# Optimization experiments

Hardware: AMD Instinct MI355X
Metric: run time of the kernel (lower is better)

## Reference

```python
import jax, jax.numpy as jnp
import numpy as np

B, S, D, H = 2, 2048, 1024, 16
DH = D // H
LN_EPS = 1e-12


def setup_inputs() -> dict:
    key = jax.random.key(0)
    ks = jax.random.split(key, 12)
    sc = 1.0 / np.sqrt(D)
    return {
        "hidden_states": jax.random.normal(ks[0], (B, S, D), jnp.float32),
        "attention_mask": jnp.zeros((B, 1, 1, S), jnp.float32),
        "Wq": jax.random.normal(ks[1], (D, D), jnp.float32) * sc,
        "bq": jnp.zeros((D,), jnp.float32),
        "Wk": jax.random.normal(ks[2], (D, D), jnp.float32) * sc,
        "bk": jnp.zeros((D,), jnp.float32),
        "Wv": jax.random.normal(ks[3], (D, D), jnp.float32) * sc,
        "bv": jnp.zeros((D,), jnp.float32),
        "Wo": jax.random.normal(ks[4], (D, D), jnp.float32) * sc,
        "bo": jnp.zeros((D,), jnp.float32),
        "ln_w": jnp.ones((D,), jnp.float32),
        "ln_b": jnp.zeros((D,), jnp.float32),
    }


def _split_heads(x):
    # [B,S,D] -> [B,H,S,DH]
    return x.reshape(B, S, H, DH).transpose(0, 2, 1, 3)


def reference(hidden_states, attention_mask, Wq, bq, Wk, bk, Wv, bv, Wo, bo, ln_w, ln_b):
    q = _split_heads(hidden_states @ Wq + bq)
    k = _split_heads(hidden_states @ Wk + bk)
    v = _split_heads(hidden_states @ Wv + bv)
    scores = jnp.einsum("bhqd,bhkd->bhqk", q, k) / np.sqrt(DH)
    scores = scores + attention_mask
    probs = jax.nn.softmax(scores, axis=-1)  # dropout prob=0 -> identity
    ctx = jnp.einsum("bhqk,bhkd->bhqd", probs, v)
    ctx = ctx.transpose(0, 2, 1, 3).reshape(B, S, D)
    # output dense + residual + LayerNorm (biased variance, per original)
    h = ctx @ Wo + bo + hidden_states
    u = h.mean(-1, keepdims=True)
    s = ((h - u) ** 2).mean(-1, keepdims=True)
    out = ln_w * ((h - u) / jnp.sqrt(s + LN_EPS)) + ln_b
    return out, probs
```

## Files before the change

### kernel.cpp

```cpp
#include <hip/hip_runtime.h>
#include <stdint.h>


typedef __attribute__((ext_vector_type(8))) short short8;
typedef __attribute__((ext_vector_type(4))) float f32x4;

__device__ __forceinline__ unsigned short f2b(float f) {
  union { float f; unsigned u; } v; v.f = f;
  unsigned u = v.u;
  return (unsigned short)((u + 0x7fffu + ((u >> 16) & 1u)) >> 16);
}

__device__ __forceinline__ float b2f(unsigned short s) {
  union { unsigned u; float f; } v;
  v.u = ((unsigned)s) << 16;
  return v.f;
}

__global__ void k_cast_hs(const float* __restrict__ x, unsigned short* __restrict__ y, int n4) {
  int i = blockIdx.x * blockDim.x + threadIdx.x;
  if (i < n4) {
    float4 v = ((const float4*)x)[i];
    ushort4 o;
    o.x = f2b(v.x); o.y = f2b(v.y); o.z = f2b(v.z); o.w = f2b(v.w);
    ((ushort4*)y)[i] = o;
  }
}

__global__ void k_transpose_cast(const float* __restrict__ Wq, const float* __restrict__ Wk,
                                 const float* __restrict__ Wv, const float* __restrict__ Wo,
                                 unsigned short* __restrict__ Tq, unsigned short* __restrict__ Tk,
                                 unsigned short* __restrict__ Tv, unsigned short* __restrict__ To) {
  __shared__ float tile[32][33];
  const float* W; unsigned short* T;
  switch (blockIdx.z) {
    case 0: W = Wq; T = Tq; break;
    case 1: W = Wk; T = Tk; break;
    case 2: W = Wv; T = Tv; break;
    default: W = Wo; T = To; break;
  }
  int n0 = blockIdx.x * 32, k0 = blockIdx.y * 32;
  int tx = threadIdx.x, ty = threadIdx.y;
#pragma unroll
  for (int j = 0; j < 4; ++j)
    tile[ty + j * 8][tx] = W[(size_t)(k0 + ty + j * 8) * 1024 + n0 + tx];
  __syncthreads();
#pragma unroll
  for (int j = 0; j < 4; ++j)
    T[(size_t)(n0 + ty + j * 8) * 1024 + k0 + tx] = f2b(tile[tx][ty + j * 8]);
}

template <int MODE>
__global__ __launch_bounds__(256) void k_gemm(const unsigned short* __restrict__ A,
                                              const unsigned short* __restrict__ Bt, int Kd,
                                              const float* __restrict__ bias,
                                              const float* __restrict__ resid,
                                              void* __restrict__ outp, float qscale) {
  __shared__ __align__(16) unsigned short Asm[128 * 32];
  __shared__ __align__(16) unsigned short Bsm[128 * 32];
  const int t = threadIdx.x, w = t >> 6, l = t & 63;
  const int m0 = blockIdx.y * 128, n0 = blockIdx.x * 128;
  const int wr = w >> 1, wc = w & 1;
  const int lr = l & 15, lg = l >> 4;

  f32x4 acc[4][4];
#pragma unroll
  for (int mi = 0; mi < 4; ++mi)
#pragma unroll
    for (int ni = 0; ni < 4; ++ni) acc[mi][ni] = (f32x4){0.f, 0.f, 0.f, 0.f};

  const int kcol = (l & 3) * 8;
  for (int kt = 0; kt < Kd / 32; ++kt) {
    const int k0 = kt * 32;
#pragma unroll
    for (int i = 0; i < 2; ++i) {
      int ra = (i * 4 + w) * 16 + (l >> 2);
      const unsigned short* ga = A + (size_t)(m0 + ra) * Kd + k0 + kcol;
      __builtin_amdgcn_global_load_lds((const __attribute__((address_space(1))) void*)ga,
                                       (__attribute__((address_space(3))) void*)((char*)Asm + (i * 4 + w) * 1024),
                                       16, 0, 0);
      const unsigned short* gb = Bt + (size_t)(n0 + ra) * Kd + k0 + kcol;
      __builtin_amdgcn_global_load_lds((const __attribute__((address_space(1))) void*)gb,
                                       (__attribute__((address_space(3))) void*)((char*)Bsm + (i * 4 + w) * 1024),
                                       16, 0, 0);
    }
    __syncthreads();
    short8 af[4], bfv[4];
#pragma unroll
    for (int mi = 0; mi < 4; ++mi)
      af[mi] = *(const short8*)&Asm[(wr * 64 + mi * 16 + lr) * 32 + lg * 8];
#pragma unroll
    for (int ni = 0; ni < 4; ++ni)
      bfv[ni] = *(const short8*)&Bsm[(wc * 64 + ni * 16 + lr) * 32 + lg * 8];
#pragma unroll
    for (int mi = 0; mi < 4; ++mi)
#pragma unroll
      for (int ni = 0; ni < 4; ++ni)
        acc[mi][ni] = __builtin_amdgcn_mfma_f32_16x16x32_bf16(af[mi], bfv[ni], acc[mi][ni], 0, 0, 0);
    __syncthreads();
  }

#pragma unroll
  for (int mi = 0; mi < 4; ++mi) {
#pragma unroll
    for (int ni = 0; ni < 4; ++ni) {
#pragma unroll
      for (int r = 0; r < 4; ++r) {
        int row = m0 + wr * 64 + mi * 16 + lg * 4 + r;
        int col = n0 + wc * 64 + ni * 16 + lr;
        float v = acc[mi][ni][r];
        if constexpr (MODE == 0) {
          v = (v + bias[col]) * qscale;
          int b = row >> 11, s = row & 2047, h = col >> 6, dh = col & 63;
          ((unsigned short*)outp)[((size_t)((b * 16 + h) * 2048 + s)) * 64 + dh] = f2b(v);
        } else if constexpr (MODE == 1) {
          v += bias[row];
          int h = row >> 6, dh = row & 63, b = col >> 11, s = col & 2047;
          ((unsigned short*)outp)[((size_t)((b * 16 + h) * 64 + dh)) * 2048 + s] = f2b(v);
        } else {
          v += bias[col] + resid[(size_t)row * 1024 + col];
          ((float*)outp)[(size_t)row * 1024 + col] = v;
        }
      }
    }
  }
}

__global__ __launch_bounds__(256, 2) void k_attn(const unsigned short* __restrict__ Q,
                                                 const unsigned short* __restrict__ K,
                                                 const unsigned short* __restrict__ VT,
                                                 const float* __restrict__ mask,
                                                 float* __restrict__ probs,
                                                 unsigned short* __restrict__ ctx) {
  __shared__ float smax[4][16];
  __shared__ float ssum[4][16];
  __shared__ __align__(16) unsigned short Pall[16][2056];
  float (*redbuf)[16][64] = (float(*)[16][64])Pall;

  const int t = threadIdx.x, w = t >> 6, l = t & 63;
  const int qb = blockIdx.x, h = blockIdx.y, b = blockIdx.z;
  const int q0 = qb * 16;
  const int lr = l & 15, lg = l >> 4;
  const size_t head = ((size_t)(b * 16 + h)) * 2048 * 64;
  const unsigned short* Qh = Q + head + (size_t)q0 * 64;
  const unsigned short* Kh = K + head;
  const unsigned short* VTh = VT + head;

  short8 aq0 = *(const short8*)(Qh + lr * 64 + lg * 8);
  short8 aq1 = *(const short8*)(Qh + lr * 64 + 32 + lg * 8);

  f32x4 sc[32];
#pragma unroll
  for (int ni = 0; ni < 32; ++ni) {
    int col = w * 512 + ni * 16 + lr;
    short8 bk0 = *(const short8*)(Kh + (size_t)col * 64 + lg * 8);
    short8 bk1 = *(const short8*)(Kh + (size_t)col * 64 + 32 + lg * 8);
    f32x4 c = (f32x4){0.f, 0.f, 0.f, 0.f};
    c = __builtin_amdgcn_mfma_f32_16x16x32_bf16(bk0, aq0, c, 0, 0, 0);
    c = __builtin_amdgcn_mfma_f32_16x16x32_bf16(bk1, aq1, c, 0, 0, 0);
    f32x4 mv = *(const f32x4*)(mask + b * 2048 + w * 512 + ni * 16 + lg * 4);
    sc[ni] = c + mv;
  }

  float vmax = -1e30f;
#pragma unroll
  for (int ni = 0; ni < 32; ++ni)
#pragma unroll
    for (int r = 0; r < 4; ++r) vmax = fmaxf(vmax, sc[ni][r]);
  vmax = fmaxf(vmax, __shfl_xor(vmax, 16));
  vmax = fmaxf(vmax, __shfl_xor(vmax, 32));
  if (l < 16) smax[w][l] = vmax;
  __syncthreads();
  float m = fmaxf(fmaxf(smax[0][lr], smax[1][lr]), fmaxf(smax[2][lr], smax[3][lr]));

  float vsum = 0.f;
#pragma unroll
  for (int ni = 0; ni < 32; ++ni)
#pragma unroll
    for (int r = 0; r < 4; ++r) {
      float p = __expf(sc[ni][r] - m);
      sc[ni][r] = p;
      vsum += p;
    }
  vsum += __shfl_xor(vsum, 16);
  vsum += __shfl_xor(vsum, 32);
  if (l < 16) ssum[w][l] = vsum;
  __syncthreads();
  float rinv = 1.f / (ssum[0][lr] + ssum[1][lr] + ssum[2][lr] + ssum[3][lr]);

#pragma unroll
  for (int ni = 0; ni < 32; ++ni) {
    float p0 = sc[ni][0] * rinv, p1 = sc[ni][1] * rinv;
    float p2 = sc[ni][2] * rinv, p3 = sc[ni][3] * rinv;
    ushort4 pk;
    pk.x = f2b(p0); pk.y = f2b(p1); pk.z = f2b(p2); pk.w = f2b(p3);
    *(ushort4*)&Pall[lr][w * 512 + ni * 16 + lg * 4] = pk;
  }
  __syncthreads();

  f32x4 cacc[4];
#pragma unroll
  for (int n = 0; n < 4; ++n) cacc[n] = (f32x4){0.f, 0.f, 0.f, 0.f};

#pragma unroll
  for (int kc = 0; kc < 16; ++kc) {
    short8 pa = *(const short8*)&Pall[lr][w * 512 + kc * 32 + lg * 8];
    size_t kg = (size_t)w * 512 + kc * 32;
#pragma unroll
    for (int n = 0; n < 4; ++n) {
      short8 bv = *(const short8*)(VTh + (size_t)(n * 16 + lr) * 2048 + kg + lg * 8);
      cacc[n] = __builtin_amdgcn_mfma_f32_16x16x32_bf16(pa, bv, cacc[n], 0, 0, 0);
    }
  }

  {
    const size_t prow0 = ((size_t)((b * 16 + h) * 2048 + q0)) * 2048;
#pragma unroll
    for (int rr = 0; rr < 4; ++rr) {
      int row = w * 4 + rr;
      float* gp = probs + prow0 + (size_t)row * 2048;
#pragma unroll
      for (int p = 0; p < 4; ++p) {
        short8 pv = *(const short8*)&Pall[row][p * 512 + l * 8];
        f32x4 o0, o1;
        o0[0] = b2f((unsigned short)pv[0]); o0[1] = b2f((unsigned short)pv[1]);
        o0[2] = b2f((unsigned short)pv[2]); o0[3] = b2f((unsigned short)pv[3]);
        o1[0] = b2f((unsigned short)pv[4]); o1[1] = b2f((unsigned short)pv[5]);
        o1[2] = b2f((unsigned short)pv[6]); o1[3] = b2f((unsigned short)pv[7]);
        f32x4* dst = (f32x4*)(gp + p * 512 + l * 8);
        __builtin_nontemporal_store(o0, dst);
        __builtin_nontemporal_store(o1, dst + 1);
      }
    }
  }
  __syncthreads();

#pragma unroll
  for (int n = 0; n < 4; ++n)
#pragma unroll
    for (int r = 0; r < 4; ++r)
      redbuf[w][lg * 4 + r][n * 16 + lr] = cacc[n][r];
  __syncthreads();

  {
    int row = t >> 4;
    int c0 = (t & 15) * 4;
    float v0 = redbuf[0][row][c0] + redbuf[1][row][c0] + redbuf[2][row][c0] + redbuf[3][row][c0];
    float v1 = redbuf[0][row][c0 + 1] + redbuf[1][row][c0 + 1] + redbuf[2][row][c0 + 1] + redbuf[3][row][c0 + 1];
    float v2 = redbuf[0][row][c0 + 2] + redbuf[1][row][c0 + 2] + redbuf[2][row][c0 + 2] + redbuf[3][row][c0 + 2];
    float v3 = redbuf[0][row][c0 + 3] + redbuf[1][row][c0 + 3] + redbuf[2][row][c0 + 3] + redbuf[3][row][c0 + 3];
    ushort4 o;
    o.x = f2b(v0); o.y = f2b(v1); o.z = f2b(v2); o.w = f2b(v3);
    *(ushort4*)(ctx + ((size_t)(b * 2048 + q0 + row)) * 1024 + h * 64 + c0) = o;
  }
}

__global__ __launch_bounds__(256) void k_ln(const float* __restrict__ hbuf, const float* __restrict__ g,
                                            const float* __restrict__ be, float* __restrict__ out) {
  __shared__ float psum[4];
  __shared__ float psq[4];
  int tok = blockIdx.x;
  int t = threadIdx.x, w = t >> 6;
  float4 v = ((const float4*)(hbuf + (size_t)tok * 1024))[t];
  float s = v.x + v.y + v.z + v.w;
  float q = v.x * v.x + v.y * v.y + v.z * v.z + v.w * v.w;
#pragma unroll
  for (int off = 32; off >= 1; off >>= 1) {
    s += __shfl_xor(s, off);
    q += __shfl_xor(q, off);
  }
  if ((t & 63) == 0) { psum[w] = s; psq[w] = q; }
  __syncthreads();
  float S = psum[0] + psum[1] + psum[2] + psum[3];
  float Qs = psq[0] + psq[1] + psq[2] + psq[3];
  float u = S * (1.f / 1024.f);
  float var = Qs * (1.f / 1024.f) - u * u;
  float rstd = rsqrtf(var + 1e-12f);
  float4 gv = ((const float4*)g)[t];
  float4 bv = ((const float4*)be)[t];
  float4 o;
  o.x = gv.x * ((v.x - u) * rstd) + bv.x;
  o.y = gv.y * ((v.y - u) * rstd) + bv.y;
  o.z = gv.z * ((v.z - u) * rstd) + bv.z;
  o.w = gv.w * ((v.w - u) * rstd) + bv.w;
  ((float4*)(out + (size_t)tok * 1024))[t] = o;
}

extern "C" void kernel_launch(void* const* d_in, const int* in_sizes, int n_in,
                              void* d_out, int out_size, void* d_ws, size_t ws_size,
                              hipStream_t stream) {
  const float* hs   = (const float*)d_in[0];
  const float* mask = (const float*)d_in[1];
  const float* Wq   = (const float*)d_in[2];
  const float* bq   = (const float*)d_in[3];
  const float* Wk   = (const float*)d_in[4];
  const float* bk   = (const float*)d_in[5];
  const float* Wv   = (const float*)d_in[6];
  const float* bv   = (const float*)d_in[7];
  const float* Wo   = (const float*)d_in[8];
  const float* bo   = (const float*)d_in[9];
  const float* lnw  = (const float*)d_in[10];
  const float* lnb  = (const float*)d_in[11];

  float* out = (float*)d_out;
  float* probs = out + (size_t)4194304;

  char* ws = (char*)d_ws;
  const size_t MB = 1u << 20;
  unsigned short* hsb = (unsigned short*)(ws + 0 * MB);
  unsigned short* TqW = (unsigned short*)(ws + 8 * MB);
  unsigned short* TkW = (unsigned short*)(ws + 10 * MB);
  unsigned short* TvW = (unsigned short*)(ws + 12 * MB);
  unsigned short* ToW = (unsigned short*)(ws + 14 * MB);
  unsigned short* Qb  = (unsigned short*)(ws + 16 * MB);
  unsigned short* Kb  = (unsigned short*)(ws + 24 * MB);
  unsigned short* VTb = (unsigned short*)(ws + 32 * MB);
  unsigned short* ctxb = (unsigned short*)(ws + 40 * MB);
  float* hbuf = (float*)(ws + 48 * MB);

  k_cast_hs<<<4096, 256, 0, stream>>>(hs, hsb, 1048576);
  k_transpose_cast<<<dim3(32, 32, 4), dim3(32, 8), 0, stream>>>(Wq, Wk, Wv, Wo, TqW, TkW, TvW, ToW);

  k_gemm<0><<<dim3(8, 32), 256, 0, stream>>>(hsb, TqW, 1024, bq, nullptr, Qb, 0.125f);
  k_gemm<0><<<dim3(8, 32), 256, 0, stream>>>(hsb, TkW, 1024, bk, nullptr, Kb, 1.0f);
  k_gemm<1><<<dim3(32, 8), 256, 0, stream>>>(TvW, hsb, 1024, bv, nullptr, VTb, 1.0f);

  k_attn<<<dim3(128, 16, 2), 256, 0, stream>>>(Qb, Kb, VTb, mask, probs, ctxb);

  k_gemm<2><<<dim3(8, 32), 256, 0, stream>>>(ctxb, ToW, 1024, bo, hs, hbuf, 1.0f);
  k_ln<<<4096, 256, 0, stream>>>(hbuf, lnw, lnb, out);
}
```

Measured before the change: 456.0 us.

## Stream P·V in staged LDS chunks to cut shared memory and raise occupancy

The attention kernel no longer keeps the full 16x2048 bf16 probability tile in LDS. Each wave in turn stages its 512-column slice into a small buffer. All waves then write that slice to the probs output and accumulate P·V for their own 16 output columns, so the cross-wave reduction buffer goes away. The launch bound rises from 2 to 8 blocks per SIMD, and the block index is remapped so neighbouring blocks span different heads and batches. This trades extra barriers and 32 packed registers per thread for much lower LDS use and higher occupancy.

```diff
diff --git a/kernel.cpp b/kernel.cpp
--- a/kernel.cpp
+++ b/kernel.cpp
@@ -126,7 +126,7 @@
   }
 }
 
-__global__ __launch_bounds__(256, 2) void k_attn(const unsigned short* __restrict__ Q,
+__global__ __launch_bounds__(256, 8) void k_attn(const unsigned short* __restrict__ Q,
                                                  const unsigned short* __restrict__ K,
                                                  const unsigned short* __restrict__ VT,
                                                  const float* __restrict__ mask,
@@ -134,11 +134,13 @@
                                                  unsigned short* __restrict__ ctx) {
   __shared__ float smax[4][16];
   __shared__ float ssum[4][16];
-  __shared__ __align__(16) unsigned short Pall[16][2056];
-  float (*redbuf)[16][64] = (float(*)[16][64])Pall;
+  __shared__ __align__(16) unsigned short Pb[16][520];
 
   const int t = threadIdx.x, w = t >> 6, l = t & 63;
-  const int qb = blockIdx.x, h = blockIdx.y, b = blockIdx.z;
+  const int i = blockIdx.x;
+  const int hp = (i & 7) * 4 + ((i >> 3) & 3);
+  const int qb = i >> 5;
+  const int h = hp & 15, b = hp >> 4;
   const int q0 = qb * 16;
   const int lr = l & 15, lg = l >> 4;
   const size_t head = ((size_t)(b * 16 + h)) * 2048 * 64;
@@ -188,70 +190,52 @@
   __syncthreads();
   float rinv = 1.f / (ssum[0][lr] + ssum[1][lr] + ssum[2][lr] + ssum[3][lr]);
 
+  ushort4 pk[32];
 #pragma unroll
   for (int ni = 0; ni < 32; ++ni) {
-    float p0 = sc[ni][0] * rinv, p1 = sc[ni][1] * rinv;
-    float p2 = sc[ni][2] * rinv, p3 = sc[ni][3] * rinv;
-    ushort4 pk;
-    pk.x = f2b(p0); pk.y = f2b(p1); pk.z = f2b(p2); pk.w = f2b(p3);
-    *(ushort4*)&Pall[lr][w * 512 + ni * 16 + lg * 4] = pk;
-  }
-  __syncthreads();
-
-  f32x4 cacc[4];
-#pragma unroll
-  for (int n = 0; n < 4; ++n) cacc[n] = (f32x4){0.f, 0.f, 0.f, 0.f};
-
-#pragma unroll
-  for (int kc = 0; kc < 16; ++kc) {
-    short8 pa = *(const short8*)&Pall[lr][w * 512 + kc * 32 + lg * 8];
-    size_t kg = (size_t)w * 512 + kc * 32;
-#pragma unroll
-    for (int n = 0; n < 4; ++n) {
-      short8 bv = *(const short8*)(VTh + (size_t)(n * 16 + lr) * 2048 + kg + lg * 8);
-      cacc[n] = __builtin_amdgcn_mfma_f32_16x16x32_bf16(pa, bv, cacc[n], 0, 0, 0);
-    }
-  }
-
-  {
-    const size_t prow0 = ((size_t)((b * 16 + h) * 2048 + q0)) * 2048;
+    pk[ni].x = f2b(sc[ni][0] * rinv);
+    pk[ni].y = f2b(sc[ni][1] * rinv);
+    pk[ni].z = f2b(sc[ni][2] * rinv);
+    pk[ni].w = f2b(sc[ni][3] * rinv);
+  }
+
+  f32x4 cacc = (f32x4){0.f, 0.f, 0.f, 0.f};
+  const size_t prow0 = ((size_t)((b * 16 + h) * 2048 + q0)) * 2048;
+
+#pragma unroll
+  for (int p = 0; p < 4; ++p) {
+    if (w == p) {
+#pragma unroll
+      for (int ni = 0; ni < 32; ++ni)
+        *(ushort4*)&Pb[lr][ni * 16 + lg * 4] = pk[ni];
+    }
+    __syncthreads();
 #pragma unroll
     for (int rr = 0; rr < 4; ++rr) {
       int row = w * 4 + rr;
-      float* gp = probs + prow0 + (size_t)row * 2048;
-#pragma unroll
-      for (int p = 0; p < 4; ++p) {
-        short8 pv = *(const short8*)&Pall[row][p * 512 + l * 8];
-        f32x4 o0, o1;
-        o0[0] = b2f((unsigned short)pv[0]); o0[1] = b2f((unsigned short)pv[1]);
-        o0[2] = b2f((unsigned short)pv[2]); o0[3] = b2f((unsigned short)pv[3]);
-        o1[0] = b2f((unsigned short)pv[4]); o1[1] = b2f((unsigned short)pv[5]);
-        o1[2] = b2f((unsigned short)pv[6]); o1[3] = b2f((unsigned short)pv[7]);
-        f32x4* dst = (f32x4*)(gp + p * 512 + l * 8);
-        __builtin_nontemporal_store(o0, dst);
-        __builtin_nontemporal_store(o1, dst + 1);
-      }
-    }
-  }
-  __syncthreads();
-
-#pragma unroll
-  for (int n = 0; n < 4; ++n)
-#pragma unroll
-    for (int r = 0; r < 4; ++r)
-      redbuf[w][lg * 4 + r][n * 16 + lr] = cacc[n][r];
-  __syncthreads();
-
-  {
-    int row = t >> 4;
-    int c0 = (t & 15) * 4;
-    float v0 = redbuf[0][row][c0] + redbuf[1][row][c0] + redbuf[2][row][c0] + redbuf[3][row][c0];
-    float v1 = redbuf[0][row][c0 + 1] + redbuf[1][row][c0 + 1] + redbuf[2][row][c0 + 1] + redbuf[3][row][c0 + 1];
-    float v2 = redbuf[0][row][c0 + 2] + redbuf[1][row][c0 + 2] + redbuf[2][row][c0 + 2] + redbuf[3][row][c0 + 2];
-    float v3 = redbuf[0][row][c0 + 3] + redbuf[1][row][c0 + 3] + redbuf[2][row][c0 + 3] + redbuf[3][row][c0 + 3];
-    ushort4 o;
-    o.x = f2b(v0); o.y = f2b(v1); o.z = f2b(v2); o.w = f2b(v3);
-    *(ushort4*)(ctx + ((size_t)(b * 2048 + q0 + row)) * 1024 + h * 64 + c0) = o;
+      short8 pv = *(const short8*)&Pb[row][l * 8];
+      f32x4 o0, o1;
+      o0[0] = b2f((unsigned short)pv[0]); o0[1] = b2f((unsigned short)pv[1]);
+      o0[2] = b2f((unsigned short)pv[2]); o0[3] = b2f((unsigned short)pv[3]);
+      o1[0] = b2f((unsigned short)pv[4]); o1[1] = b2f((unsigned short)pv[5]);
+      o1[2] = b2f((unsigned short)pv[6]); o1[3] = b2f((unsigned short)pv[7]);
+      f32x4* dst = (f32x4*)(probs + prow0 + (size_t)row * 2048 + p * 512 + l * 8);
+      __builtin_nontemporal_store(o0, dst);
+      __builtin_nontemporal_store(o1, dst + 1);
+    }
+#pragma unroll
+    for (int kc = 0; kc < 16; ++kc) {
+      short8 pa = *(const short8*)&Pb[lr][kc * 32 + lg * 8];
+      short8 bv = *(const short8*)(VTh + (size_t)(w * 16 + lr) * 2048 + p * 512 + kc * 32 + lg * 8);
+      cacc = __builtin_amdgcn_mfma_f32_16x16x32_bf16(pa, bv, cacc, 0, 0, 0);
+    }
+    __syncthreads();
+  }
+
+#pragma unroll
+  for (int r = 0; r < 4; ++r) {
+    int q = lg * 4 + r;
+    ctx[((size_t)(b * 2048 + q0 + q)) * 1024 + h * 64 + w * 16 + lr] = f2b(cacc[r]);
   }
 }
 
@@ -325,7 +309,7 @@
   k_gemm<0><<<dim3(8, 32), 256, 0, stream>>>(hsb, TkW, 1024, bk, nullptr, Kb, 1.0f);
   k_gemm<1><<<dim3(32, 8), 256, 0, stream>>>(TvW, hsb, 1024, bv, nullptr, VTb, 1.0f);
 
-  k_attn<<<dim3(128, 16, 2), 256, 0, stream>>>(Qb, Kb, VTb, mask, probs, ctxb);
+  k_attn<<<4096, 256, 0, stream>>>(Qb, Kb, VTb, mask, probs, ctxb);
 
   k_gemm<2><<<dim3(8, 32), 256, 0, stream>>>(ctxb, ToW, 1024, bo, hs, hbuf, 1.0f);
   k_ln<<<4096, 256, 0, stream>>>(hbuf, lnw, lnb, out);
```

After: 1.191 ms. 161% more time.
